# Kernel tuning notes

Measured on AMD Instinct MI355X. Metric: run time of the kernel, lower is better.

## Reference

```python
import jax, jax.numpy as jnp
import numpy as np

EPS = 1e-6      # VN nonlinearity eps
BN_EPS = 1e-5   # torch BatchNorm default eps


def setup_inputs() -> dict:
    key = jax.random.key(0)
    k1, k2, k3 = jax.random.split(key, 3)
    B, Cin, N = 8, 64, 2048
    Cout = 64
    x = jax.random.normal(k1, (B, Cin, 3, N), dtype=jnp.float32)
    # nn.Linear(in, out, bias=False) weights: [out, in], kaiming-uniform-ish scale
    s = 1.0 / np.sqrt(Cin)
    W_feat = jax.random.uniform(k2, (Cout, Cin), jnp.float32, -s, s)
    W_dir = jax.random.uniform(k3, (Cout, Cin), jnp.float32, -s, s)
    gamma = jnp.ones((Cout,), jnp.float32)
    beta = jnp.zeros((Cout,), jnp.float32)
    return {"x": x, "W_feat": W_feat, "W_dir": W_dir, "gamma": gamma, "beta": beta, "k": 10}


def _knn_idx(xf, kk):
    # xf: [B, D, N]; returns indices of kk nearest neighbors (incl. self), [B, N, kk]
    xx = jnp.sum(xf * xf, axis=1)                       # [B, N]
    inner = jnp.einsum('bdn,bdm->bnm', xf, xf)          # [B, N, N]
    pdist = 2.0 * inner - xx[:, :, None] - xx[:, None, :]  # = -||xi-xj||^2
    _, idx = jax.lax.top_k(pdist, kk)                   # largest = nearest
    return idx


def reference(x, W_feat, W_dir, gamma, beta, k):
    B, Cin, _, N = x.shape
    K = k + 1
    xf = x.reshape(B, Cin * 3, N)                       # [B, 3*Cin, N]
    idx = _knn_idx(xf, K)                               # [B, N, K]

    # gather neighbor features: [B, N, K, 3*Cin]
    xT = jnp.transpose(xf, (0, 2, 1))                   # [B, N, 3*Cin]
    feat = jax.vmap(lambda xt, id_: xt[id_])(xT, idx)   # [B, N, K, 3*Cin]
    feat = feat.reshape(B, N, K, Cin, 3)
    feat = jnp.transpose(feat, (0, 3, 4, 1, 2))         # [B, Cin, 3, N, K]

    # VN linear
    p = jnp.einsum('oc,bcdnk->bodnk', W_feat, feat)     # [B, Cout, 3, N, K]

    # VNBatchNorm (training-mode batch stats, biased var) on vector norms
    norm = jnp.sqrt(jnp.sum(p * p, axis=2))             # [B, Cout, N, K]
    mean = jnp.mean(norm, axis=(0, 2, 3))
    var = jnp.var(norm, axis=(0, 2, 3))
    norm_bn = (norm - mean[None, :, None, None]) * jax.lax.rsqrt(var + BN_EPS)[None, :, None, None]
    norm_bn = norm_bn * gamma[None, :, None, None] + beta[None, :, None, None]
    p = p / norm[:, :, None] * norm_bn[:, :, None]

    # direction + conditional vector nonlinearity
    d = jnp.einsum('oc,bcdnk->bodnk', W_dir, feat)      # [B, Cout, 3, N, K]
    dot = jnp.sum(p * d, axis=2, keepdims=True)         # [B, Cout, 1, N, K]
    d_sq = jnp.sum(d * d, axis=2, keepdims=True)
    x_out = jnp.where(dot >= 0, p, p - dot / (d_sq + EPS) * d)

    return jnp.mean(x_out, axis=-1)                     # [B, Cout, 3, N]
```

## Files before the change

kernel.cpp:

```cpp
#include <hip/hip_runtime.h>
#include <stdint.h>

#define B_   8
#define D_   192
#define N_   2048
#define KNb  11

using u32 = uint32_t;
using u16 = unsigned short;
typedef _Float16 f16;
struct alignas(8) h4 { f16 x, y, z, w; };

typedef __attribute__((ext_vector_type(8)))  short short8;
typedef __attribute__((ext_vector_type(16))) float f32x16;
typedef __attribute__((ext_vector_type(4)))  float f32x4;

__device__ __forceinline__ u16 f2bf(float f){
  union{float f; u32 i;} x; x.f = f;
  u32 r = (x.i + 0x7fffu + ((x.i >> 16) & 1u)) >> 16;
  return (u16)r;
}
__device__ __forceinline__ u32 umax32(u32 a, u32 b){ return a > b ? a : b; }
__device__ __forceinline__ u32 umin32(u32 a, u32 b){ return a < b ? a : b; }
__device__ __forceinline__ u32 med3_u32(u32 a, u32 b, u32 c){
  u32 d;
  asm("v_med3_u32 %0, %1, %2, %3" : "=v"(d) : "v"(a), "v"(b), "v"(c));
  return d;
}

__device__ __forceinline__ void sel16(const u32* __restrict__ ctp, u32* key){
  #pragma unroll
  for (int q = 0; q < 4; ++q){
    uint4 kv = *(const uint4*)(ctp + 4*q);
    u32 ks[4] = {kv.x, kv.y, kv.z, kv.w};
    #pragma unroll
    for (int j = 0; j < 4; ++j){
      u32 kk = ks[j];
      if (__any(kk > key[0])){
        #pragma unroll
        for (int s = 0; s < 9; ++s) key[s] = med3_u32(kk, key[s], key[s+1]);
        key[9] = umax32(kk, key[9]);
      }
    }
  }
}

__global__ __launch_bounds__(256) void split_kernel(const float* __restrict__ x,
                                                    short* __restrict__ Xs,
                                                    float* __restrict__ xT,
                                                    double* __restrict__ xxd){
  __shared__ float A[D_ * 32];
  const int b = blockIdx.y, tile = blockIdx.x, m0 = tile * 32, t = threadIdx.x;
  const size_t xb = (size_t)b * D_ * N_;
  #pragma unroll
  for (int q = 0; q < 24; ++q){
    int p = t + 256*q;
    int d = p >> 5, i = p & 31;
    A[d*32 + i] = x[xb + (size_t)d*N_ + m0 + i];
  }
  __syncthreads();

  {
    const int l = t & 63, wv = t >> 6;
    const int lh = l >> 5, l31 = l & 31;
    #pragma unroll
    for (int j = 0; j < 3; ++j){
      int c = j*4 + wv;
      int dbase = c*16 + lh*8;
      union{ u16 s[8]; int4 v; } u;
      #pragma unroll
      for (int q = 0; q < 8; ++q) u.s[q] = f2bf(A[(dbase + q)*32 + l31]);
      size_t P = ((size_t)b*64 + tile)*12 + c;
      *(int4*)(Xs + P*512 + l*8) = u.v;
    }
  }
  {
    const int m = t & 31, seg = t >> 5;
    float* trow = xT + ((size_t)b*N_ + m0 + m) * 192 + seg*24;
    #pragma unroll
    for (int j = 0; j < 6; ++j){
      float4 v = { A[(seg*24 + 4*j + 0)*32 + m], A[(seg*24 + 4*j + 1)*32 + m],
                   A[(seg*24 + 4*j + 2)*32 + m], A[(seg*24 + 4*j + 3)*32 + m] };
      *(float4*)(trow + 4*j) = v;
    }
  }
  if (t < 32){
    double s = 0.0;
    #pragma unroll 4
    for (int d = 0; d < D_; ++d){ double v = (double)A[d*32 + t]; s = fma(v, v, s); }
    xxd[b*N_ + m0 + t] = s;
  }
}

#define KLA   0
#define KLCT0 12288
#define KLCT1 45568
#define KLSZ  78848
__global__ __launch_bounds__(512, 4) void knn_kernel(const short* __restrict__ Xs,
                                                     const double* __restrict__ xxd,
                                                     u16* __restrict__ cand){
  __shared__ __align__(16) char smem[KLSZ];

  const int b = blockIdx.x, n0 = blockIdx.y * 32;
  const int t = threadIdx.x, lane = t & 63, w = t >> 6;
  const int l31 = lane & 31, lh = lane >> 5;
  const int mcol = w*32 + l31;
  const int selr = t >> 4, selg = t & 15;

  {
    const short* Ap = Xs + (((size_t)b*64 + (n0 >> 5)) * 12) * 512;
    int4 v = *(const int4*)(Ap + (size_t)t*8);
    *(int4*)(smem + KLA + t*16) = v;
    if (t < 256){
      int p = t + 512;
      int4 v2 = *(const int4*)(Ap + (size_t)p*8);
      *(int4*)(smem + KLA + p*16) = v2;
    }
  }
  float xxn[16];
  #pragma unroll
  for (int reg = 0; reg < 16; ++reg){
    int r = (reg & 3) + 8*(reg >> 2) + 4*lh;
    xxn[reg] = (float)xxd[b*N_ + n0 + r];
  }
  __syncthreads();

  u32 key[10];
  #pragma unroll
  for (int j = 0; j < 10; ++j) key[j] = 0u;

  for (int st = 0; st < 8; ++st){
    const int m0 = st * 256;
    const short* Bp = Xs + (((size_t)b*64 + st*8 + w) * 12) * 512 + lane*8;
    short8 pg[12];
    #pragma unroll
    for (int j = 0; j < 12; ++j) pg[j] = *(const short8*)(Bp + j*512);
    float xxs = (float)xxd[b*N_ + m0 + mcol];

    if (st > 0){
      const u32* ctp = (const u32*)(smem + ((st & 1) ? KLCT0 : KLCT1))
                       + selr*260 + selg*16;
      sel16(ctp, key);
    }

    f32x16 acc = (f32x16)0.0f;
    #pragma unroll
    for (int kc = 0; kc < 6; ++kc){
      short8 a0 = *(const short8*)(smem + KLA + (kc*2+0)*1024 + lane*16);
      short8 a1 = *(const short8*)(smem + KLA + (kc*2+1)*1024 + lane*16);
      acc = __builtin_amdgcn_mfma_f32_32x32x16_bf16(a0, pg[kc*2+0], acc, 0, 0, 0);
      acc = __builtin_amdgcn_mfma_f32_32x32x16_bf16(a1, pg[kc*2+1], acc, 0, 0, 0);
    }

    {
      u32* ctw = (u32*)(smem + ((st & 1) ? KLCT1 : KLCT0));
      const u32 midx = (u32)(m0 + mcol);
      #pragma unroll
      for (int reg = 0; reg < 16; ++reg){
        float v = fmaf(2.f, acc[reg], -(xxs + xxn[reg]));
        u32 bb = __float_as_uint(v);
        u32 kk = ((bb ^ (u32)(((int)bb >> 31) | 0x80000000)) & 0xFFFFF800u) | midx;
        int r = (reg & 3) + 8*(reg >> 2) + 4*lh;
        ctw[r*260 + mcol] = kk;
      }
    }
    __syncthreads();
  }
  {
    const u32* ctp = (const u32*)(smem + KLCT1) + selr*260 + selg*16;
    sel16(ctp, key);
  }

  {
    u32 mycand = 0u;
    #pragma unroll
    for (int s = 0; s < 16; ++s){
      u32 h = key[9];
      u32 wm = h;
      #pragma unroll
      for (int d = 1; d < 16; d <<= 1) wm = umax32(wm, __shfl_xor(wm, d, 16));
      bool win = (h == wm);
      #pragma unroll
      for (int q = 9; q > 0; --q) key[q] = win ? key[q-1] : key[q];
      key[0] = win ? 0u : key[0];
      mycand = (selg == s) ? wm : mycand;
    }
    cand[((size_t)b*N_ + n0 + selr)*16 + selg] = (u16)(mycand & 2047u);
  }
}

__global__ __launch_bounds__(256, 3) void refine_kernel(const float* __restrict__ xT,
                                                        const u16* __restrict__ cand,
                                                        const double* __restrict__ xxd,
                                                        int* __restrict__ idxout,
                                                        int* __restrict__ cnt){
  const int wv = threadIdx.x >> 6, ln = threadIdx.x & 63;
  const int b = blockIdx.x & 7;
  const int n = (blockIdx.x >> 3) * 4 + wv;
  const int g = b * N_ + n;
  const int c = ln >> 2, part = ln & 3;
  const int m = (int)cand[(size_t)g*16 + c] & 2047;
  const f32x4* pn = (const f32x4*)(xT + ((size_t)b*N_ + n)*192 + part*48);
  const f32x4* pm = (const f32x4*)(xT + ((size_t)b*N_ + m)*192 + part*48);
  f32x4 an[12], am[12];
  #pragma unroll
  for (int j = 0; j < 12; ++j) an[j] = pn[j];
  #pragma unroll
  for (int j = 0; j < 12; ++j) am[j] = pm[j];
  asm volatile(""
    : "+v"(an[0]), "+v"(an[1]), "+v"(an[2]),  "+v"(an[3]),  "+v"(an[4]),  "+v"(an[5]),
      "+v"(an[6]), "+v"(an[7]), "+v"(an[8]),  "+v"(an[9]),  "+v"(an[10]), "+v"(an[11]),
      "+v"(am[0]), "+v"(am[1]), "+v"(am[2]),  "+v"(am[3]),  "+v"(am[4]),  "+v"(am[5]),
      "+v"(am[6]), "+v"(am[7]), "+v"(am[8]),  "+v"(am[9]),  "+v"(am[10]), "+v"(am[11]));
  __builtin_amdgcn_sched_barrier(0);

  double s0 = 0.0, s1 = 0.0, s2 = 0.0, s3 = 0.0;
  #pragma unroll
  for (int j = 0; j < 12; j += 4){
    s0 = fma((double)an[j+0][0], (double)am[j+0][0], s0);
    s0 = fma((double)an[j+0][1], (double)am[j+0][1], s0);
    s0 = fma((double)an[j+0][2], (double)am[j+0][2], s0);
    s0 = fma((double)an[j+0][3], (double)am[j+0][3], s0);
    s1 = fma((double)an[j+1][0], (double)am[j+1][0], s1);
    s1 = fma((double)an[j+1][1], (double)am[j+1][1], s1);
    s1 = fma((double)an[j+1][2], (double)am[j+1][2], s1);
    s1 = fma((double)an[j+1][3], (double)am[j+1][3], s1);
    s2 = fma((double)an[j+2][0], (double)am[j+2][0], s2);
    s2 = fma((double)an[j+2][1], (double)am[j+2][1], s2);
    s2 = fma((double)an[j+2][2], (double)am[j+2][2], s2);
    s2 = fma((double)an[j+2][3], (double)am[j+2][3], s2);
    s3 = fma((double)an[j+3][0], (double)am[j+3][0], s3);
    s3 = fma((double)an[j+3][1], (double)am[j+3][1], s3);
    s3 = fma((double)an[j+3][2], (double)am[j+3][2], s3);
    s3 = fma((double)an[j+3][3], (double)am[j+3][3], s3);
  }
  double s = (s0 + s1) + (s2 + s3);
  s += __shfl_down(s, 2, 64);
  s += __shfl_down(s, 1, 64);
  double v = 2.0*s - xxd[b*N_ + n] - xxd[b*N_ + m];
  int rank = 0;
  #pragma unroll
  for (int q = 0; q < 16; ++q){
    double vq = __shfl(v, q*4, 64);
    int    mq = __shfl(m, q*4, 64);
    bool beat = (vq > v) || ((vq == v) && (mq < m));
    rank += beat ? 1 : 0;
  }
  if (part == 0 && rank < KNb){
    idxout[(size_t)g*KNb + rank] = m;
    atomicAdd(&cnt[b*N_ + m], 1);
  }
}

__global__ __launch_bounds__(256) void project_kernel(const float* __restrict__ xT,
                                                      const float* __restrict__ Wf,
                                                      const float* __restrict__ Wd,
                                                      h4* __restrict__ P0h,
                                                      h4* __restrict__ D0h){
  __shared__ float A[16 * 192];
  const int b = blockIdx.x, m0 = blockIdx.y * 16, t = threadIdx.x;
  const int l = t & 63, wv = t >> 6;
  const int half = l >> 5;
  const int c = (wv & 1)*32 + (l & 31);
  const int mg = wv >> 1;

  float wfh[32], wdh[32];
  #pragma unroll
  for (int q = 0; q < 8; ++q){
    float4 uf = *(const float4*)(Wf + c*64 + half*32 + q*4);
    wfh[q*4+0]=uf.x; wfh[q*4+1]=uf.y; wfh[q*4+2]=uf.z; wfh[q*4+3]=uf.w;
    float4 ud = *(const float4*)(Wd + c*64 + half*32 + q*4);
    wdh[q*4+0]=ud.x; wdh[q*4+1]=ud.y; wdh[q*4+2]=ud.z; wdh[q*4+3]=ud.w;
  }
  {
    const float4* src = (const float4*)(xT + ((size_t)b*N_ + m0)*192);
    float4* dst = (float4*)A;
    #pragma unroll
    for (int j = 0; j < 3; ++j) dst[t + 256*j] = src[t + 256*j];
  }
  __syncthreads();

  for (int i = 0; i < 8; ++i){
    int m = mg*8 + i;
    const float4* row = (const float4*)(A + m*192 + half*96);
    float p[3] = {0.f,0.f,0.f}, qv[3] = {0.f,0.f,0.f};
    #pragma unroll
    for (int v4 = 0; v4 < 24; ++v4){
      float4 f = row[v4];
      const int e = v4*4;
      p [(e+0)%3] = fmaf(wfh[(e+0)/3], f.x, p [(e+0)%3]);
      qv[(e+0)%3] = fmaf(wdh[(e+0)/3], f.x, qv[(e+0)%3]);
      p [(e+1)%3] = fmaf(wfh[(e+1)/3], f.y, p [(e+1)%3]);
      qv[(e+1)%3] = fmaf(wdh[(e+1)/3], f.y, qv[(e+1)%3]);
      p [(e+2)%3] = fmaf(wfh[(e+2)/3], f.z, p [(e+2)%3]);
      qv[(e+2)%3] = fmaf(wdh[(e+2)/3], f.z, qv[(e+2)%3]);
      p [(e+3)%3] = fmaf(wfh[(e+3)/3], f.w, p [(e+3)%3]);
      qv[(e+3)%3] = fmaf(wdh[(e+3)/3], f.w, qv[(e+3)%3]);
    }
    float o0 = __shfl_xor(p[0], 32, 64), o1 = __shfl_xor(p[1], 32, 64);
    float o2 = __shfl_xor(p[2], 32, 64);
    float u0 = __shfl_xor(qv[0], 32, 64), u1 = __shfl_xor(qv[1], 32, 64);
    float u2 = __shfl_xor(qv[2], 32, 64);
    if (half == 0){
      float t0 = p[0] + o0, t1 = p[1] + o1, t2 = p[2] + o2;
      float r0 = qv[0] + u0, r1 = qv[1] + u1, r2 = qv[2] + u2;
      float nrm = sqrtf(t0*t0 + t1*t1 + t2*t2);
      float dsq = r0*r0 + r1*r1 + r2*r2;
      size_t base = ((size_t)b*N_ + m0 + m)*64 + c;
      h4 vp; vp.x = (f16)t0; vp.y = (f16)t1; vp.z = (f16)t2; vp.w = (f16)nrm;
      h4 vd; vd.x = (f16)r0; vd.y = (f16)r1; vd.z = (f16)r2; vd.w = (f16)dsq;
      P0h[base] = vp;
      D0h[base] = vd;
    }
  }
}

__global__ __launch_bounds__(256) void stats_kernel(const h4* __restrict__ P0h,
                                                    const int* __restrict__ cnt,
                                                    float* __restrict__ gs){
  const int b = blockIdx.x >> 6;
  const int chunk = blockIdx.x & 63;
  const int w = threadIdx.x >> 6, c = threadIdx.x & 63;
  float s = 0.f, s2 = 0.f;
  const int mbase = chunk*32 + w*8;
  for (int i = 0; i < 8; ++i){
    int m = mbase + i;
    float wt = (float)cnt[b*N_ + m];
    float nv = (float)P0h[((size_t)b*N_ + m)*64 + c].w;
    s  = fmaf(wt, nv, s);
    s2 = fmaf(wt*nv, nv, s2);
  }
  __shared__ float red[8][64];
  red[w][c] = s; red[4+w][c] = s2;
  __syncthreads();
  if (w == 0) atomicAdd(&gs[c],    red[0][c]+red[1][c]+red[2][c]+red[3][c]);
  if (w == 1) atomicAdd(&gs[64+c], red[4][c]+red[5][c]+red[6][c]+red[7][c]);
}

__global__ __launch_bounds__(512) void out_kernel(const h4* __restrict__ P0h, const h4* __restrict__ D0h,
                                                  const int* __restrict__ idxin, const float* __restrict__ gs,
                                                  const float* __restrict__ gamma, const float* __restrict__ beta,
                                                  float* __restrict__ outp){
  __shared__ float res[16 * 193];
  const int b  = blockIdx.x;
  const int n0 = blockIdx.y * 16;
  const int t = threadIdx.x, w = t >> 6, c = t & 63;
  const float Ninv = 1.f / (float)(B_*N_*KNb);
  float mean = gs[c] * Ninv;
  float var  = gs[64+c] * Ninv - mean*mean;
  float istd = rsqrtf(var + 1e-5f);
  float sa = istd * gamma[c];
  float be = beta[c];
  const float kinv = 1.f/11.f;
  for (int i = 0; i < 2; ++i){
    int row = w*2 + i;
    int n = n0 + row;
    const int* ip = idxin + ((size_t)b*N_ + n)*KNb;
    float a0=0, a1=0, a2=0;
    #pragma unroll
    for (int k = 0; k < KNb; ++k){
      int m = ip[k] & 2047;
      size_t base = ((size_t)b*N_ + m)*64 + c;
      h4 P  = P0h[base];
      h4 Dv = D0h[base];
      float pw = (float)P.w;
      float nb = (pw - mean)*sa + be;
      float sc = nb / pw;
      float p0 = (float)P.x*sc, p1 = (float)P.y*sc, p2 = (float)P.z*sc;
      float d0 = (float)Dv.x, d1 = (float)Dv.y, d2 = (float)Dv.z;
      float dot = p0*d0 + p1*d1 + p2*d2;
      float f = (dot >= 0.f) ? 0.f : dot / ((float)Dv.w + 1e-6f);
      a0 += p0 - f*d0; a1 += p1 - f*d1; a2 += p2 - f*d2;
    }
    res[row*193 + 3*c + 0] = a0*kinv;
    res[row*193 + 3*c + 1] = a1*kinv;
    res[row*193 + 3*c + 2] = a2*kinv;
  }
  __syncthreads();
  {
    int p = t;
    #pragma unroll
    for (int j = 0; j < 2; ++j){
      if (p < 768){
        int cdim = p >> 2, nq = p & 3;
        float4 v = { res[(nq*4 + 0)*193 + cdim], res[(nq*4 + 1)*193 + cdim],
                     res[(nq*4 + 2)*193 + cdim], res[(nq*4 + 3)*193 + cdim] };
        *(float4*)(outp + ((size_t)b*192 + cdim)*N_ + n0 + nq*4) = v;
      }
      p += 512;
    }
  }
}

extern "C" void kernel_launch(void* const* d_in, const int* in_sizes, int n_in,
                              void* d_out, int out_size, void* d_ws, size_t ws_size,
                              hipStream_t stream){
  const float* x     = (const float*)d_in[0];
  const float* Wf    = (const float*)d_in[1];
  const float* Wd    = (const float*)d_in[2];
  const float* gamma = (const float*)d_in[3];
  const float* beta  = (const float*)d_in[4];
  float* outp = (float*)d_out;

  char* ws = (char*)d_ws;
  int*    idx  = (int*)   (ws);
  int*    cnt  = (int*)   (ws + 720896);
  float*  gs   = (float*) (ws + 786432);
  h4*     P0h  = (h4*)    (ws + 1048576);
  h4*     D0h  = (h4*)    (ws + 9437184);
  short*  Xs   = (short*) (ws + 1048576);
  double* xxd  = (double*)(ws + 13631488);
  u16*    cand = (u16*)   (ws + 13762560);
  float*  xT   = (float*) (ws + 17825792);

  hipMemsetAsync(cnt, 0, 66048, stream);
  split_kernel  <<<dim3(64, 8),  256, 0, stream>>>(x, Xs, xT, xxd);
  knn_kernel    <<<dim3(8, 64),  512, 0, stream>>>(Xs, xxd, cand);
  refine_kernel <<<4096,         256, 0, stream>>>(xT, cand, xxd, idx, cnt);
  project_kernel<<<dim3(8, 128), 256, 0, stream>>>(xT, Wf, Wd, P0h, D0h);
  stats_kernel  <<<512,          256, 0, stream>>>(P0h, cnt, gs);
  out_kernel    <<<dim3(8, 128), 512, 0, stream>>>(P0h, D0h, idx, gs, gamma, beta, outp);
}
```

Measured before the change: 217.5 us.

## Retile kNN distance kernel to 16-row blocks with 16x16x32 MFMA

Switches the kNN distance tile from 32 query rows per block using 32x32x16 MFMA to 16 rows per block using 16x16x32 MFMA. The bf16 packing in the split kernel is relaid to match, and each selection thread now scans 8 candidates per stage instead of 16. This doubles the grid to 1024 blocks and shrinks shared memory so more blocks can be resident, which is meant to improve occupancy and parallelism. In exchange, every block rereads the full key matrix, so global/L2 traffic for the B operand doubles, and only half the threads do selection.

Measured after the change: 226.7 us. 4.2% more time.

```diff
diff --git a/kernel.cpp b/kernel.cpp
--- a/kernel.cpp
+++ b/kernel.cpp
@@ -12,7 +12,6 @@
 struct alignas(8) h4 { f16 x, y, z, w; };
 
 typedef __attribute__((ext_vector_type(8)))  short short8;
-typedef __attribute__((ext_vector_type(16))) float f32x16;
 typedef __attribute__((ext_vector_type(4)))  float f32x4;
 
 __device__ __forceinline__ u16 f2bf(float f){
@@ -28,9 +27,9 @@
   return d;
 }
 
-__device__ __forceinline__ void sel16(const u32* __restrict__ ctp, u32* key){
-  #pragma unroll
-  for (int q = 0; q < 4; ++q){
+__device__ __forceinline__ void sel8(const u32* __restrict__ ctp, u32* key){
+  #pragma unroll
+  for (int q = 0; q < 2; ++q){
     uint4 kv = *(const uint4*)(ctp + 4*q);
     u32 ks[4] = {kv.x, kv.y, kv.z, kv.w};
     #pragma unroll
@@ -62,15 +61,17 @@
 
   {
     const int l = t & 63, wv = t >> 6;
-    const int lh = l >> 5, l31 = l & 31;
+    const int r16 = l & 15, kg = l >> 4;
     #pragma unroll
     for (int j = 0; j < 3; ++j){
-      int c = j*4 + wv;
-      int dbase = c*16 + lh*8;
+      int p = j*4 + wv;
+      int sub = p / 6, c = p % 6;
+      int dbase = c*32 + kg*8;
+      int row = sub*16 + r16;
       union{ u16 s[8]; int4 v; } u;
       #pragma unroll
-      for (int q = 0; q < 8; ++q) u.s[q] = f2bf(A[(dbase + q)*32 + l31]);
-      size_t P = ((size_t)b*64 + tile)*12 + c;
+      for (int q = 0; q < 8; ++q) u.s[q] = f2bf(A[(dbase + q)*32 + row]);
+      size_t P = ((size_t)b*128 + blockIdx.x*2 + sub)*6 + c;
       *(int4*)(Xs + P*512 + l*8) = u.v;
     }
   }
@@ -93,85 +94,75 @@
 }
 
 #define KLA   0
-#define KLCT0 12288
-#define KLCT1 45568
-#define KLSZ  78848
+#define KLCT0 6144
+#define KLCT1 14592
+#define KLSZ  23040
 __global__ __launch_bounds__(512, 4) void knn_kernel(const short* __restrict__ Xs,
                                                      const double* __restrict__ xxd,
                                                      u16* __restrict__ cand){
   __shared__ __align__(16) char smem[KLSZ];
 
-  const int b = blockIdx.x, n0 = blockIdx.y * 32;
+  const int b = blockIdx.x, n0 = blockIdx.y * 16;
   const int t = threadIdx.x, lane = t & 63, w = t >> 6;
-  const int l31 = lane & 31, lh = lane >> 5;
-  const int mcol = w*32 + l31;
+  const int l15 = lane & 15;
   const int selr = t >> 4, selg = t & 15;
 
-  {
-    const short* Ap = Xs + (((size_t)b*64 + (n0 >> 5)) * 12) * 512;
-    int4 v = *(const int4*)(Ap + (size_t)t*8);
-    *(int4*)(smem + KLA + t*16) = v;
-    if (t < 256){
-      int p = t + 512;
-      int4 v2 = *(const int4*)(Ap + (size_t)p*8);
-      *(int4*)(smem + KLA + p*16) = v2;
-    }
-  }
-  float xxn[16];
-  #pragma unroll
-  for (int reg = 0; reg < 16; ++reg){
-    int r = (reg & 3) + 8*(reg >> 2) + 4*lh;
-    xxn[reg] = (float)xxd[b*N_ + n0 + r];
-  }
+  if (t < 384){
+    const short* Ap = Xs + ((size_t)(b*128 + blockIdx.y) * 6) * 512;
+    int p = t >> 6, l = t & 63;
+    int4 v = *(const int4*)(Ap + (size_t)p*512 + l*8);
+    *(int4*)(smem + KLA + p*1024 + l*16) = v;
+  }
+  float xxn[4];
+  #pragma unroll
+  for (int reg = 0; reg < 4; ++reg)
+    xxn[reg] = (float)xxd[b*N_ + n0 + (lane >> 4)*4 + reg];
   __syncthreads();
 
   u32 key[10];
   #pragma unroll
   for (int j = 0; j < 10; ++j) key[j] = 0u;
 
-  for (int st = 0; st < 8; ++st){
-    const int m0 = st * 256;
-    const short* Bp = Xs + (((size_t)b*64 + st*8 + w) * 12) * 512 + lane*8;
-    short8 pg[12];
-    #pragma unroll
-    for (int j = 0; j < 12; ++j) pg[j] = *(const short8*)(Bp + j*512);
-    float xxs = (float)xxd[b*N_ + m0 + mcol];
-
-    if (st > 0){
+  for (int st = 0; st < 16; ++st){
+    const int m0s = st * 128;
+    const short* Bp = Xs + ((size_t)(b*128 + st*8 + w) * 6) * 512 + lane*8;
+    short8 pg[6];
+    #pragma unroll
+    for (int j = 0; j < 6; ++j) pg[j] = *(const short8*)(Bp + j*512);
+    float xxs = (float)xxd[b*N_ + m0s + w*16 + l15];
+
+    if (st > 0 && t < 256){
       const u32* ctp = (const u32*)(smem + ((st & 1) ? KLCT0 : KLCT1))
-                       + selr*260 + selg*16;
-      sel16(ctp, key);
-    }
-
-    f32x16 acc = (f32x16)0.0f;
+                       + selr*132 + selg*8;
+      sel8(ctp, key);
+    }
+
+    f32x4 acc = (f32x4)0.0f;
     #pragma unroll
     for (int kc = 0; kc < 6; ++kc){
-      short8 a0 = *(const short8*)(smem + KLA + (kc*2+0)*1024 + lane*16);
-      short8 a1 = *(const short8*)(smem + KLA + (kc*2+1)*1024 + lane*16);
-      acc = __builtin_amdgcn_mfma_f32_32x32x16_bf16(a0, pg[kc*2+0], acc, 0, 0, 0);
-      acc = __builtin_amdgcn_mfma_f32_32x32x16_bf16(a1, pg[kc*2+1], acc, 0, 0, 0);
+      short8 a0 = *(const short8*)(smem + KLA + kc*1024 + lane*16);
+      acc = __builtin_amdgcn_mfma_f32_16x16x32_bf16(a0, pg[kc], acc, 0, 0, 0);
     }
 
     {
       u32* ctw = (u32*)(smem + ((st & 1) ? KLCT1 : KLCT0));
-      const u32 midx = (u32)(m0 + mcol);
+      const int ctcol = w*16 + l15;
+      const u32 midx = (u32)(m0s + ctcol);
       #pragma unroll
-      for (int reg = 0; reg < 16; ++reg){
+      for (int reg = 0; reg < 4; ++reg){
         float v = fmaf(2.f, acc[reg], -(xxs + xxn[reg]));
         u32 bb = __float_as_uint(v);
         u32 kk = ((bb ^ (u32)(((int)bb >> 31) | 0x80000000)) & 0xFFFFF800u) | midx;
-        int r = (reg & 3) + 8*(reg >> 2) + 4*lh;
-        ctw[r*260 + mcol] = kk;
+        int r = (lane >> 4)*4 + reg;
+        ctw[r*132 + ctcol] = kk;
       }
     }
     __syncthreads();
   }
-  {
-    const u32* ctp = (const u32*)(smem + KLCT1) + selr*260 + selg*16;
-    sel16(ctp, key);
-  }
-
-  {
+  if (t < 256){
+    const u32* ctp = (const u32*)(smem + KLCT1) + selr*132 + selg*8;
+    sel8(ctp, key);
+
     u32 mycand = 0u;
     #pragma unroll
     for (int s = 0; s < 16; ++s){
@@ -415,7 +406,7 @@
 
   hipMemsetAsync(cnt, 0, 66048, stream);
   split_kernel  <<<dim3(64, 8),  256, 0, stream>>>(x, Xs, xT, xxd);
-  knn_kernel    <<<dim3(8, 64),  512, 0, stream>>>(Xs, xxd, cand);
+  knn_kernel    <<<dim3(8, 128), 512, 0, stream>>>(Xs, xxd, cand);
   refine_kernel <<<4096,         256, 0, stream>>>(xT, cand, xxd, idx, cnt);
   project_kernel<<<dim3(8, 128), 256, 0, stream>>>(xT, Wf, Wd, P0h, D0h);
   stats_kernel  <<<512,          256, 0, stream>>>(P0h, cnt, gs);
```
